# Optimization experiments

Hardware: AMD Instinct MI355X
Metric: run time of the kernel (lower is better)

Reference implementation:

```python
import jax, jax.numpy as jnp
import numpy as np

N_CTX = 4096
D_MODEL = 2048
D_HEAD = 128


def setup_inputs() -> dict:
    key = jax.random.key(0)
    k1, k2, k3, k4 = jax.random.split(key, 4)
    x = jax.random.normal(k1, (N_CTX, D_MODEL), dtype=jnp.float32)
    # torch nn.Linear weights are [out, in]; kept in that layout.
    Wk = jax.random.normal(k2, (D_HEAD, D_MODEL), dtype=jnp.float32) * (1.0 / np.sqrt(D_MODEL))
    Wq = jax.random.normal(k3, (D_HEAD, D_MODEL), dtype=jnp.float32) * (1.0 / np.sqrt(D_MODEL))
    W2 = jax.random.normal(k4, (D_MODEL, D_MODEL), dtype=jnp.float32) * (1.0 / np.sqrt(D_MODEL))
    return {"x": x, "Wk": Wk, "Wq": Wq, "W2": W2}


def reference(x, Wk, Wq, W2):
    # Faithful to the torch module: no 1/sqrt(d_head) scaling, V = x itself.
    n = x.shape[0]
    q = x @ Wq.T                     # [n, d_head]
    k = x @ Wk.T                     # [n, d_head]
    scores = q @ k.T                 # [n, n]
    # causal mask: strictly-upper-triangular entries -> -inf
    causal = jnp.tril(jnp.ones((n, n), dtype=bool))
    scores = jnp.where(causal, scores, -jnp.inf)
    attn = jax.nn.softmax(scores, axis=1)  # [n, n]
    out = attn @ x                   # [n, d_model] (V is the raw input)
    return out @ W2.T                # [n, d_model]
```

## Files before the change

### kernel.cpp

```cpp
#include <hip/hip_runtime.h>

#define NCTX 4096
#define DMODEL 2048
#define DHEAD 128

typedef _Float16 f16;
typedef f16 f16x8 __attribute__((ext_vector_type(8)));
typedef float f32x4 __attribute__((ext_vector_type(4)));
typedef unsigned short u16;
typedef u16 u16x8 __attribute__((ext_vector_type(8)));

__device__ __forceinline__ u16 f2h(float f) {
  union { f16 h; u16 u; } v; v.h = (f16)f; return v.u;
}
__device__ __forceinline__ float h2f(u16 u) {
  union { u16 u; f16 h; } v; v.u = u; return (float)v.h;
}

__device__ __forceinline__ void gl_lds16(const void* g, void* l) {
  __builtin_amdgcn_global_load_lds((const __attribute__((address_space(1))) void*)g,
                                   (__attribute__((address_space(3))) void*)l, 16, 0, 0);
}

__device__ __forceinline__ void splitH4(float4 v, ushort4& h, ushort4& l) {
  h.x = f2h(v.x); l.x = f2h(v.x - h2f(h.x));
  h.y = f2h(v.y); l.y = f2h(v.y - h2f(h.y));
  h.z = f2h(v.z); l.z = f2h(v.z - h2f(h.z));
  h.w = f2h(v.w); l.w = f2h(v.w - h2f(h.w));
}

__global__ __launch_bounds__(256) void prep_all(const float* __restrict__ x,
                                                const float* __restrict__ Wq,
                                                const float* __restrict__ Wk,
                                                const float* __restrict__ W2,
                                                u16* __restrict__ xh, u16* __restrict__ xl,
                                                u16* __restrict__ Wf, u16* __restrict__ W2f,
                                                u16* __restrict__ XT) {
  __shared__ float tile[64][65];
  int b = blockIdx.x;
  int t = threadIdx.x;
  if (b < 2048) {
    int mb = (b >> 5) * 64, db = (b & 31) * 64;
    int tx = t & 15, ty = t >> 4;
#pragma unroll
    for (int rr = 0; rr < 4; ++rr) {
      int row = rr * 16 + ty;
      float4 v = *(const float4*)(x + (size_t)(mb + row) * DMODEL + db + tx * 4);
      ushort4 h, l; splitH4(v, h, l);
      size_t gi = ((size_t)(mb + row) * DMODEL + db) / 4 + tx;
      ((ushort4*)xh)[gi] = h; ((ushort4*)xl)[gi] = l;
      tile[row][tx * 4 + 0] = v.x; tile[row][tx * 4 + 1] = v.y;
      tile[row][tx * 4 + 2] = v.z; tile[row][tx * 4 + 3] = v.w;
    }
    __syncthreads();
#pragma unroll
    for (int rr = 0; rr < 4; ++rr) {
      int r = (t >> 4) * 4 + rr;
      int c0 = (t & 15) * 4;
      ushort4 o;
      o.x = f2h(tile[c0 + 0][r]); o.y = f2h(tile[c0 + 1][r]);
      o.z = f2h(tile[c0 + 2][r]); o.w = f2h(tile[c0 + 3][r]);
      *(ushort4*)(XT + (size_t)(db + r) * NCTX + mb + c0) = o;
    }
  } else if (b < 2560) {
    int wk = (b >= 2304);
    int i = (b - (wk ? 2304 : 2048)) * 256 + t;
    const float* W = wk ? Wk : Wq;
    size_t off = wk ? ((size_t)DHEAD * DMODEL / 4) : 0;
    float4 v = ((const float4*)W)[i];
    ushort4 o;
    o.x = f2h(v.x); o.y = f2h(v.y); o.z = f2h(v.z); o.w = f2h(v.w);
    ((ushort4*)Wf)[off + i] = o;
  } else {
    int i = (b - 2560) * 256 + t;
    float4 v = ((const float4*)W2)[i];
    ushort4 o;
    o.x = f2h(v.x); o.y = f2h(v.y); o.z = f2h(v.z); o.w = f2h(v.w);
    ((ushort4*)W2f)[i] = o;
  }
}

__global__ __launch_bounds__(256) void reduce8h(const u16* __restrict__ P,
                                                u16* __restrict__ out, int n8) {
  int i = blockIdx.x * 256 + threadIdx.x;
  if (i >= n8) return;
  float s[8] = {};
#pragma unroll
  for (int z = 0; z < 8; ++z) {
    u16x8 v = ((const u16x8*)P)[(size_t)z * n8 + i];
#pragma unroll
    for (int k = 0; k < 8; ++k) s[k] += h2f(v[k]);
  }
  u16x8 o;
#pragma unroll
  for (int k = 0; k < 8; ++k) o[k] = f2h(s[k]);
  ((u16x8*)out)[i] = o;
}

__global__ __launch_bounds__(256) void reduce_c2(const u16* __restrict__ P,
                                                 u16* __restrict__ out, size_t cs) {
  int row = 2048 + blockIdx.x;
  int t = threadIdx.x;
  size_t base = (size_t)row * DMODEL + t * 8;
  u16x8 a = *(const u16x8*)(P + base);
  u16x8 b = *(const u16x8*)(P + cs + base);
  u16x8 o;
#pragma unroll
  for (int k = 0; k < 8; ++k) o[k] = f2h(h2f(a[k]) + h2f(b[k]));
  *(u16x8*)(out + base) = o;
}

__global__ __launch_bounds__(256) void softmax_wave(const float* __restrict__ S,
                                                    u16* __restrict__ P) {
  int t = threadIdx.x;
  int lane = t & 63, w = t >> 6;
  int row = blockIdx.x * 4 + w;
  const float* srow = S + (size_t)row * NCTX;
  int len = row + 1;
  int jmax = ((row >> 7) + 1) << 7;
  float4 v[16];
  float mx = -3.0e38f;
#pragma unroll
  for (int k = 0; k < 16; ++k) {
    int j = k * 256 + lane * 4;
    if (j < jmax) {
      float4 x = *(const float4*)(srow + j);
      x.x = (j + 0 < len) ? x.x : -3.0e38f;
      x.y = (j + 1 < len) ? x.y : -3.0e38f;
      x.z = (j + 2 < len) ? x.z : -3.0e38f;
      x.w = (j + 3 < len) ? x.w : -3.0e38f;
      v[k] = x;
      mx = fmaxf(mx, fmaxf(fmaxf(x.x, x.y), fmaxf(x.z, x.w)));
    }
  }
#pragma unroll
  for (int o = 32; o > 0; o >>= 1) mx = fmaxf(mx, __shfl_xor(mx, o, 64));
  float sum = 0.f;
#pragma unroll
  for (int k = 0; k < 16; ++k) {
    int j = k * 256 + lane * 4;
    if (j < jmax) {
      float4 x = v[k];
      x.x = (j + 0 < len) ? __expf(x.x - mx) : 0.f;
      x.y = (j + 1 < len) ? __expf(x.y - mx) : 0.f;
      x.z = (j + 2 < len) ? __expf(x.z - mx) : 0.f;
      x.w = (j + 3 < len) ? __expf(x.w - mx) : 0.f;
      v[k] = x;
      sum += x.x + x.y + x.z + x.w;
    }
  }
#pragma unroll
  for (int o = 32; o > 0; o >>= 1) sum += __shfl_xor(sum, o, 64);
  float inv = 1.0f / sum;
  u16* prow = P + (size_t)row * NCTX;
#pragma unroll
  for (int k = 0; k < 16; ++k) {
    int j = k * 256 + lane * 4;
    if (j < jmax) {
      float4 x = v[k];
      ushort4 o4;
      o4.x = f2h(x.x * inv); o4.y = f2h(x.y * inv);
      o4.z = f2h(x.z * inv); o4.w = f2h(x.w * inv);
      *(ushort4*)(prow + j) = o4;
    }
  }
}

__global__ __launch_bounds__(256, 4) void gemm_scores(const u16* __restrict__ A,
                                                      const u16* __restrict__ B,
                                                      float* __restrict__ C) {
  int q = blockIdx.x;
  int bm = (int)((sqrtf(8.0f * (float)q + 1.0f) - 1.0f) * 0.5f);
  while ((bm + 1) * (bm + 2) / 2 <= q) ++bm;
  while (bm * (bm + 1) / 2 > q) --bm;
  int bn = q - bm * (bm + 1) / 2;
  __shared__ __align__(16) u16 As[128 * 64];
  __shared__ __align__(16) u16 Bs[128 * 64];
  int t = threadIdx.x;
  int lane = t & 63, w = t >> 6;
  int m0 = bm * 128, n0 = bn * 128;
  int wm = (w >> 1) * 64, wn = (w & 1) * 64;
  int mfrag = lane & 15, quad = lane >> 4;
  int srow = t >> 3, schunk = t & 7;
  int rsw = mfrag & 7;
  f32x4 acc[4][4] = {};
#pragma unroll
  for (int kt = 0; kt < 128; kt += 64) {
#pragma unroll
    for (int p = 0; p < 4; ++p) {
      int row = p * 32 + srow;
      int gsc = schunk ^ (row & 7);
      gl_lds16(A + (size_t)(m0 + row) * 256 + kt + gsc * 8, As + (size_t)(p * 256 + t) * 8);
      gl_lds16(B + (size_t)(n0 + row) * 256 + kt + gsc * 8, Bs + (size_t)(p * 256 + t) * 8);
    }
    __syncthreads();
#pragma unroll
    for (int ks = 0; ks < 2; ++ks) {
      int c0 = ((ks * 4 + quad) ^ rsw) * 8;
      f16x8 af[4], bfr[4];
#pragma unroll
      for (int i = 0; i < 4; ++i)
        af[i] = *(const f16x8*)(As + (wm + i * 16 + mfrag) * 64 + c0);
#pragma unroll
      for (int j = 0; j < 4; ++j)
        bfr[j] = *(const f16x8*)(Bs + (wn + j * 16 + mfrag) * 64 + c0);
#pragma unroll
      for (int i = 0; i < 4; ++i)
#pragma unroll
        for (int j = 0; j < 4; ++j)
          acc[i][j] = __builtin_amdgcn_mfma_f32_16x16x32_f16(af[i], bfr[j], acc[i][j], 0, 0, 0);
    }
    __syncthreads();
  }
#pragma unroll
  for (int i = 0; i < 4; ++i)
#pragma unroll
    for (int j = 0; j < 4; ++j)
#pragma unroll
      for (int rr = 0; rr < 4; ++rr) {
        int row = m0 + wm + i * 16 + quad * 4 + rr;
        int col = n0 + wn + j * 16 + mfrag;
        C[(size_t)row * NCTX + col] = acc[i][j][rr];
      }
}

__global__ __launch_bounds__(256, 4) void gemm_f16_p(const u16* __restrict__ A,
                                                     const u16* __restrict__ B,
                                                     float* __restrict__ C,
                                                     int lda, int ldb, int ldc,
                                                     int K) {
  int bm = blockIdx.x, bn = blockIdx.y;
  __shared__ __align__(16) u16 As[128 * 64];
  __shared__ __align__(16) u16 Bs[128 * 64];
  int t = threadIdx.x;
  int lane = t & 63, w = t >> 6;
  int m0 = bm * 128, n0 = bn * 128;
  int wm = (w >> 1) * 64, wn = (w & 1) * 64;
  int mfrag = lane & 15, quad = lane >> 4;
  int srow = t >> 3, schunk = t & 7;
  int rsw = mfrag & 7;
  f32x4 acc[4][4] = {};
  for (int kt = 0; kt < K; kt += 64) {
#pragma unroll
    for (int p = 0; p < 4; ++p) {
      int row = p * 32 + srow;
      int gsc = schunk ^ (row & 7);
      gl_lds16(A + (size_t)(m0 + row) * lda + kt + gsc * 8, As + (size_t)(p * 256 + t) * 8);
      gl_lds16(B + (size_t)(n0 + row) * ldb + kt + gsc * 8, Bs + (size_t)(p * 256 + t) * 8);
    }
    __syncthreads();
#pragma unroll
    for (int ks = 0; ks < 2; ++ks) {
      int c0 = ((ks * 4 + quad) ^ rsw) * 8;
      f16x8 af[4], bfr[4];
#pragma unroll
      for (int i = 0; i < 4; ++i)
        af[i] = *(const f16x8*)(As + (wm + i * 16 + mfrag) * 64 + c0);
#pragma unroll
      for (int j = 0; j < 4; ++j)
        bfr[j] = *(const f16x8*)(Bs + (wn + j * 16 + mfrag) * 64 + c0);
#pragma unroll
      for (int i = 0; i < 4; ++i)
#pragma unroll
        for (int j = 0; j < 4; ++j)
          acc[i][j] = __builtin_amdgcn_mfma_f32_16x16x32_f16(af[i], bfr[j], acc[i][j], 0, 0, 0);
    }
    __syncthreads();
  }
#pragma unroll
  for (int i = 0; i < 4; ++i)
#pragma unroll
    for (int j = 0; j < 4; ++j)
#pragma unroll
      for (int rr = 0; rr < 4; ++rr) {
        int row = m0 + wm + i * 16 + quad * 4 + rr;
        int col = n0 + wn + j * 16 + mfrag;
        C[(size_t)row * ldc + col] = acc[i][j][rr];
      }
}

__global__ __launch_bounds__(256, 4) void gemm_attnx(const u16* __restrict__ A,
                                                     const u16* __restrict__ B,
                                                     u16* __restrict__ C,
                                                     u16* __restrict__ Cf,
                                                     size_t chunkStride) {
  int b = blockIdx.x;
  int s = b >> 8, c = b & 255;
  int r = (s == 0) ? c : (s == 1) ? (511 - c) : (512 + c);
  int bm, bn, kc;
  if (r < 272) {
    bm = 15 + (r >> 4); bn = r & 15; kc = 0;
  } else if (r < 288) {
    bm = 31; bn = r - 272; kc = 1;
  } else {
    int g = (r - 288) >> 5, j = (r - 288) & 31;
    int k = 15 - g;
    if (j < 16) { bm = k - 1; bn = j; kc = 0; }
    else        { bm = 15 + k; bn = j - 16; kc = 1; }
  }
  int kEnd = (bm + 1) * 128;
  if (kEnd > NCTX) kEnd = NCTX;
  int kStart = kc * 2048;
  int kStop = kStart + 2048 < kEnd ? kStart + 2048 : kEnd;
  __shared__ __align__(16) u16 As[128 * 64];
  __shared__ __align__(16) u16 Bs[128 * 64];
  int t = threadIdx.x;
  int lane = t & 63, w = t >> 6;
  int m0 = bm * 128, n0 = bn * 128;
  int wm = (w >> 1) * 64, wn = (w & 1) * 64;
  int mfrag = lane & 15, quad = lane >> 4;
  int srow = t >> 3, schunk = t & 7;
  int rsw = mfrag & 7;
  f32x4 acc[4][4] = {};
  for (int kt = kStart; kt < kStop; kt += 64) {
#pragma unroll
    for (int p = 0; p < 4; ++p) {
      int row = p * 32 + srow;
      int gsc = schunk ^ (row & 7);
      gl_lds16(A + (size_t)(m0 + row) * NCTX + kt + gsc * 8, As + (size_t)(p * 256 + t) * 8);
      gl_lds16(B + (size_t)(n0 + row) * NCTX + kt + gsc * 8, Bs + (size_t)(p * 256 + t) * 8);
    }
    __syncthreads();
#pragma unroll
    for (int ks = 0; ks < 2; ++ks) {
      int c0 = ((ks * 4 + quad) ^ rsw) * 8;
      f16x8 af[4], bfr[4];
#pragma unroll
      for (int i = 0; i < 4; ++i)
        af[i] = *(const f16x8*)(As + (wm + i * 16 + mfrag) * 64 + c0);
#pragma unroll
      for (int j = 0; j < 4; ++j)
        bfr[j] = *(const f16x8*)(Bs + (wn + j * 16 + mfrag) * 64 + c0);
#pragma unroll
      for (int i = 0; i < 4; ++i)
#pragma unroll
        for (int j = 0; j < 4; ++j)
          acc[i][j] = __builtin_amdgcn_mfma_f32_16x16x32_f16(af[i], bfr[j], acc[i][j], 0, 0, 0);
    }
    __syncthreads();
  }
  u16* Cc = (kc == 0 && kEnd <= 2048) ? Cf : (C + (size_t)kc * chunkStride);
#pragma unroll
  for (int i = 0; i < 4; ++i)
#pragma unroll
    for (int j = 0; j < 4; ++j)
#pragma unroll
      for (int rr = 0; rr < 4; ++rr) {
        int row = m0 + wm + i * 16 + quad * 4 + rr;
        int col = n0 + wn + j * 16 + mfrag;
        Cc[(size_t)row * DMODEL + col] = f2h(acc[i][j][rr]);
      }
}

__global__ __launch_bounds__(256, 3) void gemm_f16x2_p(const u16* __restrict__ Ah,
                                                       const u16* __restrict__ Al,
                                                       const u16* __restrict__ B,
                                                       u16* __restrict__ C,
                                                       int lda, int ldb, int ldc,
                                                       int K, int KC, size_t chunkStride) {
  int bm = blockIdx.x, bn = blockIdx.y, kc = blockIdx.z;
  int kStart = kc * KC;
  int kStop = kStart + KC < K ? kStart + KC : K;
  __shared__ __align__(16) u16 Ash[128 * 64];
  __shared__ __align__(16) u16 Asl[128 * 64];
  __shared__ __align__(16) u16 Bs[128 * 64];
  int t = threadIdx.x;
  int lane = t & 63, w = t >> 6;
  int m0 = bm * 128, n0 = bn * 128;
  int wm = (w >> 1) * 64, wn = (w & 1) * 64;
  int mfrag = lane & 15, quad = lane >> 4;
  int srow = t >> 3, schunk = t & 7;
  int rsw = mfrag & 7;
  f32x4 acc[4][4] = {};
  for (int kt = kStart; kt < kStop; kt += 64) {
#pragma unroll
    for (int p = 0; p < 4; ++p) {
      int row = p * 32 + srow;
      int gsc = schunk ^ (row & 7);
      size_t aoff = (size_t)(m0 + row) * lda + kt + gsc * 8;
      size_t loff = (size_t)(p * 256 + t) * 8;
      gl_lds16(Ah + aoff, Ash + loff);
      gl_lds16(Al + aoff, Asl + loff);
      gl_lds16(B + (size_t)(n0 + row) * ldb + kt + gsc * 8, Bs + loff);
    }
    __syncthreads();
#pragma unroll
    for (int ks = 0; ks < 2; ++ks) {
      int c0 = ((ks * 4 + quad) ^ rsw) * 8;
      f16x8 a0[4], bfr[4];
#pragma unroll
      for (int j = 0; j < 4; ++j)
        bfr[j] = *(const f16x8*)(Bs + (wn + j * 16 + mfrag) * 64 + c0);
#pragma unroll
      for (int i = 0; i < 4; ++i)
        a0[i] = *(const f16x8*)(Ash + (wm + i * 16 + mfrag) * 64 + c0);
#pragma unroll
      for (int i = 0; i < 4; ++i)
#pragma unroll
        for (int j = 0; j < 4; ++j)
          acc[i][j] = __builtin_amdgcn_mfma_f32_16x16x32_f16(a0[i], bfr[j], acc[i][j], 0, 0, 0);
#pragma unroll
      for (int i = 0; i < 4; ++i)
        a0[i] = *(const f16x8*)(Asl + (wm + i * 16 + mfrag) * 64 + c0);
#pragma unroll
      for (int i = 0; i < 4; ++i)
#pragma unroll
        for (int j = 0; j < 4; ++j)
          acc[i][j] = __builtin_amdgcn_mfma_f32_16x16x32_f16(a0[i], bfr[j], acc[i][j], 0, 0, 0);
    }
    __syncthreads();
  }
  u16* Cc = C + (size_t)kc * chunkStride;
#pragma unroll
  for (int i = 0; i < 4; ++i)
#pragma unroll
    for (int j = 0; j < 4; ++j)
#pragma unroll
      for (int rr = 0; rr < 4; ++rr) {
        int row = m0 + wm + i * 16 + quad * 4 + rr;
        int col = n0 + wn + j * 16 + mfrag;
        Cc[(size_t)row * ldc + col] = f2h(acc[i][j][rr]);
      }
}

extern "C" void kernel_launch(void* const* d_in, const int* in_sizes, int n_in,
                              void* d_out, int out_size, void* d_ws, size_t ws_size,
                              hipStream_t stream) {
  const float* x  = (const float*)d_in[0];
  const float* Wk = (const float*)d_in[1];
  const float* Wq = (const float*)d_in[2];
  const float* W2 = (const float*)d_in[3];

  char* ws = (char*)d_ws;
  const size_t MB = 1024 * 1024;
  u16*   QKf  = (u16*)  (ws + 0);
  u16*   Wf   = (u16*)  (ws + 2 * MB);
  u16*   xT   = (u16*)  (ws + 3 * MB);
  u16*   W2f  = (u16*)  (ws + 19 * MB);
  u16*   outb = (u16*)  (ws + 27 * MB);
  u16*   attn = (u16*)  (ws + 43 * MB);
  u16*   xh   = (u16*)  (ws + 75 * MB);
  u16*   xl   = (u16*)  (ws + 91 * MB);
  u16*   QKp  = (u16*)  (ws + 107 * MB);
  float* S    = (float*)(ws + 75 * MB);
  u16*   Ph   = (u16*)  (ws + 75 * MB);

  const int QKN8 = NCTX * 256 / 8;
  const size_t CS = (size_t)NCTX * DMODEL;

  prep_all<<<6656, 256, 0, stream>>>(x, Wq, Wk, W2, xh, xl, Wf, W2f, xT);

  gemm_f16x2_p<<<dim3(NCTX / 128, 2, 8), 256, 0, stream>>>(
      xh, xl, Wf, QKp, DMODEL, DMODEL, 256, DMODEL, 256, (size_t)NCTX * 256);
  reduce8h<<<(QKN8 + 255) / 256, 256, 0, stream>>>(QKp, QKf, QKN8);

  gemm_scores<<<528, 256, 0, stream>>>(QKf, QKf + DHEAD, S);
  softmax_wave<<<1024, 256, 0, stream>>>(S, attn);

  gemm_attnx<<<768, 256, 0, stream>>>(attn, xT, Ph, outb, CS);
  reduce_c2<<<2048, 256, 0, stream>>>(Ph, outb, CS);

  gemm_f16_p<<<dim3(NCTX / 128, DMODEL / 128), 256, 0, stream>>>(
      outb, W2f, (float*)d_out, DMODEL, DMODEL, DMODEL, DMODEL);
}
```

Measured before the change: 234.2 us.

## Split hi/lo QK projection across k-chunks and use 2D grid for scores

The QK projection kernel, which loaded both hi and lo halves of x per tile, is replaced by a kernel where each z-slice handles either the hi or lo half over a 512-wide K range. This drops LDS use to two tiles so occupancy can rise, and keeps the 8-way partial-sum reduction unchanged. The causal scores GEMM now launches a full 32x32 grid with upper-triangle blocks exiting early, ordered from the largest rows first, instead of decoding a triangular index with sqrt. The scores change adds launch of empty blocks in exchange for simpler indexing and different scheduling order.

```diff
diff --git a/kernel.cpp b/kernel.cpp
--- a/kernel.cpp
+++ b/kernel.cpp
@@ -169,11 +169,8 @@
 __global__ __launch_bounds__(256, 4) void gemm_scores(const u16* __restrict__ A,
                                                       const u16* __restrict__ B,
                                                       float* __restrict__ C) {
-  int q = blockIdx.x;
-  int bm = (int)((sqrtf(8.0f * (float)q + 1.0f) - 1.0f) * 0.5f);
-  while ((bm + 1) * (bm + 2) / 2 <= q) ++bm;
-  while (bm * (bm + 1) / 2 > q) --bm;
-  int bn = q - bm * (bm + 1) / 2;
+  int bm = 31 - blockIdx.x, bn = blockIdx.y;
+  if (bn > bm) return;
   __shared__ __align__(16) u16 As[128 * 64];
   __shared__ __align__(16) u16 Bs[128 * 64];
   int t = threadIdx.x;
@@ -221,6 +218,64 @@
         int row = m0 + wm + i * 16 + quad * 4 + rr;
         int col = n0 + wn + j * 16 + mfrag;
         C[(size_t)row * NCTX + col] = acc[i][j][rr];
+      }
+}
+
+__global__ __launch_bounds__(256, 4) void gemm_qk(const u16* __restrict__ Ah,
+                                                  const u16* __restrict__ Al,
+                                                  const u16* __restrict__ B,
+                                                  u16* __restrict__ C) {
+  int bm = blockIdx.x, bn = blockIdx.y, kc = blockIdx.z;
+  const u16* A = (kc < 4) ? Ah : Al;
+  int kStart = (kc & 3) * 512;
+  int kStop = kStart + 512;
+  __shared__ __align__(16) u16 As[128 * 64];
+  __shared__ __align__(16) u16 Bs[128 * 64];
+  int t = threadIdx.x;
+  int lane = t & 63, w = t >> 6;
+  int m0 = bm * 128, n0 = bn * 128;
+  int wm = (w >> 1) * 64, wn = (w & 1) * 64;
+  int mfrag = lane & 15, quad = lane >> 4;
+  int srow = t >> 3, schunk = t & 7;
+  int rsw = mfrag & 7;
+  f32x4 acc[4][4] = {};
+  for (int kt = kStart; kt < kStop; kt += 64) {
+#pragma unroll
+    for (int p = 0; p < 4; ++p) {
+      int row = p * 32 + srow;
+      int gsc = schunk ^ (row & 7);
+      gl_lds16(A + (size_t)(m0 + row) * DMODEL + kt + gsc * 8, As + (size_t)(p * 256 + t) * 8);
+      gl_lds16(B + (size_t)(n0 + row) * DMODEL + kt + gsc * 8, Bs + (size_t)(p * 256 + t) * 8);
+    }
+    __syncthreads();
+#pragma unroll
+    for (int ks = 0; ks < 2; ++ks) {
+      int c0 = ((ks * 4 + quad) ^ rsw) * 8;
+      f16x8 af[4], bfr[4];
+#pragma unroll
+      for (int i = 0; i < 4; ++i)
+        af[i] = *(const f16x8*)(As + (wm + i * 16 + mfrag) * 64 + c0);
+#pragma unroll
+      for (int j = 0; j < 4; ++j)
+        bfr[j] = *(const f16x8*)(Bs + (wn + j * 16 + mfrag) * 64 + c0);
+#pragma unroll
+      for (int i = 0; i < 4; ++i)
+#pragma unroll
+        for (int j = 0; j < 4; ++j)
+          acc[i][j] = __builtin_amdgcn_mfma_f32_16x16x32_f16(af[i], bfr[j], acc[i][j], 0, 0, 0);
+    }
+    __syncthreads();
+  }
+  u16* Cc = C + (size_t)kc * ((size_t)NCTX * 256);
+#pragma unroll
+  for (int i = 0; i < 4; ++i)
+#pragma unroll
+    for (int j = 0; j < 4; ++j)
+#pragma unroll
+      for (int rr = 0; rr < 4; ++rr) {
+        int row = m0 + wm + i * 16 + quad * 4 + rr;
+        int col = n0 + wn + j * 16 + mfrag;
+        Cc[(size_t)row * 256 + col] = f2h(acc[i][j][rr]);
       }
 }
 
@@ -352,77 +407,6 @@
       }
 }
 
-__global__ __launch_bounds__(256, 3) void gemm_f16x2_p(const u16* __restrict__ Ah,
-                                                       const u16* __restrict__ Al,
-                                                       const u16* __restrict__ B,
-                                                       u16* __restrict__ C,
-                                                       int lda, int ldb, int ldc,
-                                                       int K, int KC, size_t chunkStride) {
-  int bm = blockIdx.x, bn = blockIdx.y, kc = blockIdx.z;
-  int kStart = kc * KC;
-  int kStop = kStart + KC < K ? kStart + KC : K;
-  __shared__ __align__(16) u16 Ash[128 * 64];
-  __shared__ __align__(16) u16 Asl[128 * 64];
-  __shared__ __align__(16) u16 Bs[128 * 64];
-  int t = threadIdx.x;
-  int lane = t & 63, w = t >> 6;
-  int m0 = bm * 128, n0 = bn * 128;
-  int wm = (w >> 1) * 64, wn = (w & 1) * 64;
-  int mfrag = lane & 15, quad = lane >> 4;
-  int srow = t >> 3, schunk = t & 7;
-  int rsw = mfrag & 7;
-  f32x4 acc[4][4] = {};
-  for (int kt = kStart; kt < kStop; kt += 64) {
-#pragma unroll
-    for (int p = 0; p < 4; ++p) {
-      int row = p * 32 + srow;
-      int gsc = schunk ^ (row & 7);
-      size_t aoff = (size_t)(m0 + row) * lda + kt + gsc * 8;
-      size_t loff = (size_t)(p * 256 + t) * 8;
-      gl_lds16(Ah + aoff, Ash + loff);
-      gl_lds16(Al + aoff, Asl + loff);
-      gl_lds16(B + (size_t)(n0 + row) * ldb + kt + gsc * 8, Bs + loff);
-    }
-    __syncthreads();
-#pragma unroll
-    for (int ks = 0; ks < 2; ++ks) {
-      int c0 = ((ks * 4 + quad) ^ rsw) * 8;
-      f16x8 a0[4], bfr[4];
-#pragma unroll
-      for (int j = 0; j < 4; ++j)
-        bfr[j] = *(const f16x8*)(Bs + (wn + j * 16 + mfrag) * 64 + c0);
-#pragma unroll
-      for (int i = 0; i < 4; ++i)
-        a0[i] = *(const f16x8*)(Ash + (wm + i * 16 + mfrag) * 64 + c0);
-#pragma unroll
-      for (int i = 0; i < 4; ++i)
-#pragma unroll
-        for (int j = 0; j < 4; ++j)
-          acc[i][j] = __builtin_amdgcn_mfma_f32_16x16x32_f16(a0[i], bfr[j], acc[i][j], 0, 0, 0);
-#pragma unroll
-      for (int i = 0; i < 4; ++i)
-        a0[i] = *(const f16x8*)(Asl + (wm + i * 16 + mfrag) * 64 + c0);
-#pragma unroll
-      for (int i = 0; i < 4; ++i)
-#pragma unroll
-        for (int j = 0; j < 4; ++j)
-          acc[i][j] = __builtin_amdgcn_mfma_f32_16x16x32_f16(a0[i], bfr[j], acc[i][j], 0, 0, 0);
-    }
-    __syncthreads();
-  }
-  u16* Cc = C + (size_t)kc * chunkStride;
-#pragma unroll
-  for (int i = 0; i < 4; ++i)
-#pragma unroll
-    for (int j = 0; j < 4; ++j)
-#pragma unroll
-      for (int rr = 0; rr < 4; ++rr) {
-        int row = m0 + wm + i * 16 + quad * 4 + rr;
-        int col = n0 + wn + j * 16 + mfrag;
-        Cc[(size_t)row * ldc + col] = f2h(acc[i][j][rr]);
-      }
-}
-
 extern "C" void kernel_launch(void* const* d_in, const int* in_sizes, int n_in,
                               void* d_out, int out_size, void* d_ws, size_t ws_size,
                               hipStream_t stream) {
@@ -450,11 +434,10 @@
 
   prep_all<<<6656, 256, 0, stream>>>(x, Wq, Wk, W2, xh, xl, Wf, W2f, xT);
 
-  gemm_f16x2_p<<<dim3(NCTX / 128, 2, 8), 256, 0, stream>>>(
-      xh, xl, Wf, QKp, DMODEL, DMODEL, 256, DMODEL, 256, (size_t)NCTX * 256);
+  gemm_qk<<<dim3(NCTX / 128, 2, 8), 256, 0, stream>>>(xh, xl, Wf, QKp);
   reduce8h<<<(QKN8 + 255) / 256, 256, 0, stream>>>(QKp, QKf, QKN8);
 
-  gemm_scores<<<528, 256, 0, stream>>>(QKf, QKf + DHEAD, S);
+  gemm_scores<<<dim3(32, 32), 256, 0, stream>>>(QKf, QKf + DHEAD, S);
   softmax_wave<<<1024, 256, 0, stream>>>(S, attn);
 
   gemm_attnx<<<768, 256, 0, stream>>>(attn, xT, Ph, outb, CS);
```

Result: faster. 226.5 us (-3.3%).
